# Performance work log

Hardware: AMD Instinct MI355X
Metric: run time of the kernel (lower is better)

## Reference

```python
import jax, jax.numpy as jnp
import numpy as np

N_NODES = 50000
ALPHA = 0.1
K_ITERS = 10


def setup_inputs() -> dict:
    key = jax.random.key(0)
    ks = jax.random.split(key, 6)
    x = jax.random.normal(ks[0], (N_NODES, 256), dtype=jnp.float32)
    edge_index = jax.random.randint(ks[1], (2, 800000), 0, N_NODES, dtype=jnp.int64)
    # Glorot-ish scaled weights
    W1 = jax.random.normal(ks[2], (256, 128), dtype=jnp.float32) * (1.0 / np.sqrt(256))
    b1 = jnp.zeros((128,), dtype=jnp.float32)
    W3 = jax.random.normal(ks[3], (128, 64), dtype=jnp.float32) * (1.0 / np.sqrt(128))
    b3 = jnp.zeros((64,), dtype=jnp.float32)
    return {"x": x, "edge_index": edge_index, "W1": W1, "b1": b1, "W3": W3, "b3": b3}


def _gcn_norm(edge_index, n_nodes):
    # Add self-loops, then symmetric normalization D^{-1/2} (A+I) D^{-1/2}
    loops = jnp.arange(n_nodes, dtype=edge_index.dtype)
    src = jnp.concatenate([edge_index[0], loops])
    dst = jnp.concatenate([edge_index[1], loops])
    deg = jax.ops.segment_sum(jnp.ones_like(dst, dtype=jnp.float32), dst,
                              num_segments=n_nodes)
    dinv = jnp.where(deg > 0, jax.lax.rsqrt(deg), 0.0)
    w = dinv[src] * dinv[dst]  # [E + N]
    return src, dst, w


def _propagate(h, src, dst, w, n_nodes):
    # out[dst] += w * h[src]  (gather -> scale -> scatter-add)
    msgs = w[:, None] * h[src]
    return jax.ops.segment_sum(msgs, dst, num_segments=n_nodes)


def reference(x, edge_index, W1, b1, W3, b3):
    n = x.shape[0]
    src, dst, w = _gcn_norm(edge_index, n)

    # GCNConv 1: linear then normalized propagation
    h = _propagate(x @ W1 + b1, src, dst, w, n)

    # APPNP: K iterations of h = (1-alpha)*A_hat h + alpha*h0 (eval: no edge dropout)
    h0 = h

    def step(hc, _):
        hn = (1.0 - ALPHA) * _propagate(hc, src, dst, w, n) + ALPHA * h0
        return hn, None

    h, _ = jax.lax.scan(step, h, None, length=K_ITERS)

    # GCNConv 2
    out = _propagate(h @ W3 + b3, src, dst, w, n)
    return out
```

## Files before the change

kernel.cpp:

```cpp
#include <hip/hip_runtime.h>

#define NN 50000
#define NE 800000
#define NTP (NE + 8 * NN)


__global__ void zero_deg_kernel(int* deg) {
  int v = blockIdx.x * 256 + threadIdx.x;
  if (v < NN) deg[v] = 0;
}

__global__ void count_deg_kernel(const int* __restrict__ edst, int* __restrict__ deg) {
  int i = blockIdx.x * 256 + threadIdx.x;
  if (i < NE) atomicAdd(&deg[edst[i]], 1);
}

__global__ void dinv_kernel(const int* __restrict__ deg, float* __restrict__ dinv) {
  int v = blockIdx.x * 256 + threadIdx.x;
  if (v < NN) dinv[v] = rsqrtf((float)(deg[v] + 1));
}

__device__ __forceinline__ int pdeg_of(int deg) {
  return ((deg + 8) >> 3) << 3;
}

__global__ __launch_bounds__(1024) void scan1_kernel(const int* __restrict__ deg,
                                                     int* __restrict__ incl,
                                                     int* __restrict__ bsum) {
  __shared__ int sd[1024];
  int gid = blockIdx.x * 1024 + threadIdx.x;
  int v = (gid < NN) ? pdeg_of(deg[gid]) : 0;
  sd[threadIdx.x] = v;
  __syncthreads();
  for (int off = 1; off < 1024; off <<= 1) {
    int t = (threadIdx.x >= off) ? sd[threadIdx.x - off] : 0;
    __syncthreads();
    sd[threadIdx.x] += t;
    __syncthreads();
  }
  if (gid < NN) incl[gid] = sd[threadIdx.x];
  if (threadIdx.x == 1023) bsum[blockIdx.x] = sd[1023];
}

__global__ void scan2_kernel(int* bsum, int nb) {
  if (threadIdx.x == 0 && blockIdx.x == 0) {
    int run = 0;
    for (int i = 0; i < nb; ++i) { int t = bsum[i]; bsum[i] = run; run += t; }
  }
}

__global__ void scan3_kernel(const int* __restrict__ deg, const int* __restrict__ incl,
                             const int* __restrict__ bsum, int* __restrict__ offs,
                             int* __restrict__ cursor) {
  int v = blockIdx.x * 256 + threadIdx.x;
  if (v >= NN) return;
  int pd = pdeg_of(deg[v]);
  int o = bsum[v >> 10] + incl[v] - pd;
  offs[v] = o;
  cursor[v] = o;
  if (v == NN - 1) offs[NN] = o + pd;
}

__global__ void zero_edges_kernel(int2* edges) {
  int i = blockIdx.x * 256 + threadIdx.x;
  if (i < NTP) edges[i] = make_int2(0, 0);
}

#define FILL_STRIDE (832 * 256)
__global__ void fill_kernel(const int* __restrict__ esrc, const int* __restrict__ edst,
                            const float* __restrict__ dinv, int* __restrict__ cursor,
                            int2* __restrict__ edges) {
  int i = blockIdx.x * 256 + threadIdx.x;
  for (; i < NE + NN; i += FILL_STRIDE) {
    int s, d;
    if (i < NE) { s = esrc[i]; d = edst[i]; }
    else        { s = d = i - NE; }
    int p = atomicAdd(&cursor[d], 1);
    int2 e;
    e.x = s;
    e.y = __float_as_int(dinv[s] * dinv[d]);
    edges[p] = e;
  }
}

__global__ void rowsum_kernel(const int* __restrict__ offs, const int2* __restrict__ edges,
                              float* __restrict__ rowsum) {
  int v = blockIdx.x * 256 + threadIdx.x;
  if (v >= NN) return;
  float s = 0.f;
  int e1 = offs[v + 1];
  for (int e = offs[v]; e < e1; ++e) s += __int_as_float(edges[e].y);
  rowsum[v] = s;
}


__global__ void w13_kernel(const float* __restrict__ W1, const float* __restrict__ W3,
                           float* __restrict__ W13) {
  int idx = blockIdx.x * 256 + threadIdx.x;
  if (idx >= 256 * 64) return;
  int r = idx >> 6, c = idx & 63;
  float acc = 0.f;
  for (int k = 0; k < 128; ++k) acc += W1[r * 128 + k] * W3[k * 64 + c];
  W13[idx] = acc;
}

__global__ void b13_kernel(const float* __restrict__ b1, const float* __restrict__ W3,
                           float* __restrict__ b13) {
  int c = threadIdx.x;
  if (c >= 64) return;
  float acc = 0.f;
  for (int k = 0; k < 128; ++k) acc += b1[k] * W3[k * 64 + c];
  b13[c] = acc;
}


template <int K>
__global__ __launch_bounds__(512) void gemm64_kernel(const float* __restrict__ A,
                                                     const float* __restrict__ W,
                                                     const float* __restrict__ bias,
                                                     float* __restrict__ out, int M) {
  __shared__ float xs[64][36];
  __shared__ float ws[32][64];

  int tid = threadIdx.x;
  int tc = tid & 15;
  int tr = tid >> 4;
  int row0 = blockIdx.x * 64;

  int xr = tid >> 3, xk = (tid & 7) * 4;
  int wk = tid >> 4, wc = (tid & 15) * 4;

  float acc[2][4] = {};

  for (int kc = 0; kc < K; kc += 32) {
    {
      int row = row0 + xr;
      float4 v = make_float4(0.f, 0.f, 0.f, 0.f);
      if (row < M) v = *reinterpret_cast<const float4*>(&A[(size_t)row * K + kc + xk]);
      *reinterpret_cast<float4*>(&xs[xr][xk]) = v;
      *reinterpret_cast<float4*>(&ws[wk][wc]) =
          *reinterpret_cast<const float4*>(&W[(size_t)(kc + wk) * 64 + wc]);
    }
    __syncthreads();
#pragma unroll
    for (int kk = 0; kk < 32; kk += 4) {
      float4 xv[2], wv[4];
#pragma unroll
      for (int r = 0; r < 2; ++r)
        xv[r] = *reinterpret_cast<const float4*>(&xs[tr * 2 + r][kk]);
#pragma unroll
      for (int q = 0; q < 4; ++q)
        wv[q] = *reinterpret_cast<const float4*>(&ws[kk + q][tc * 4]);
#pragma unroll
      for (int r = 0; r < 2; ++r) {
        acc[r][0] += xv[r].x * wv[0].x + xv[r].y * wv[1].x + xv[r].z * wv[2].x + xv[r].w * wv[3].x;
        acc[r][1] += xv[r].x * wv[0].y + xv[r].y * wv[1].y + xv[r].z * wv[2].y + xv[r].w * wv[3].y;
        acc[r][2] += xv[r].x * wv[0].z + xv[r].y * wv[1].z + xv[r].z * wv[2].z + xv[r].w * wv[3].z;
        acc[r][3] += xv[r].x * wv[0].w + xv[r].y * wv[1].w + xv[r].z * wv[2].w + xv[r].w * wv[3].w;
      }
    }
    __syncthreads();
  }

  float4 bv = *reinterpret_cast<const float4*>(&bias[tc * 4]);
#pragma unroll
  for (int r = 0; r < 2; ++r) {
    int row = row0 + tr * 2 + r;
    if (row < M) {
      float4 o;
      o.x = acc[r][0] + bv.x;
      o.y = acc[r][1] + bv.y;
      o.z = acc[r][2] + bv.z;
      o.w = acc[r][3] + bv.w;
      *reinterpret_cast<float4*>(&out[(size_t)row * 64 + tc * 4]) = o;
    }
  }
}


template <int MODE>
__global__ __launch_bounds__(256) void prop64_kernel(const float* __restrict__ hin,
                                                     const float* __restrict__ h0,
                                                     float* __restrict__ out,
                                                     const int* __restrict__ offs,
                                                     const int2* __restrict__ edges,
                                                     const float* __restrict__ rowsum,
                                                     const float* __restrict__ b3) {
  int node = blockIdx.x * 16 + (threadIdx.x >> 4);
  if (node >= NN) return;
  int f = (threadIdx.x & 15) * 4;
  const float* __restrict__ hb = hin + f;

  int e = offs[node];
  int e1 = offs[node + 1];
  float ax = 0.f, ay = 0.f, az = 0.f, aw = 0.f;

  for (; e < e1; e += 8) {
    int4 m01 = *reinterpret_cast<const int4*>(edges + e);
    int4 m23 = *reinterpret_cast<const int4*>(edges + e + 2);
    int4 m45 = *reinterpret_cast<const int4*>(edges + e + 4);
    int4 m67 = *reinterpret_cast<const int4*>(edges + e + 6);
    float4 v0 = *reinterpret_cast<const float4*>(hb + (size_t)m01.x * 64);
    float4 v1 = *reinterpret_cast<const float4*>(hb + (size_t)m01.z * 64);
    float4 v2 = *reinterpret_cast<const float4*>(hb + (size_t)m23.x * 64);
    float4 v3 = *reinterpret_cast<const float4*>(hb + (size_t)m23.z * 64);
    float4 v4 = *reinterpret_cast<const float4*>(hb + (size_t)m45.x * 64);
    float4 v5 = *reinterpret_cast<const float4*>(hb + (size_t)m45.z * 64);
    float4 v6 = *reinterpret_cast<const float4*>(hb + (size_t)m67.x * 64);
    float4 v7 = *reinterpret_cast<const float4*>(hb + (size_t)m67.z * 64);
    float w0 = __int_as_float(m01.y), w1 = __int_as_float(m01.w);
    float w2 = __int_as_float(m23.y), w3 = __int_as_float(m23.w);
    float w4 = __int_as_float(m45.y), w5 = __int_as_float(m45.w);
    float w6 = __int_as_float(m67.y), w7 = __int_as_float(m67.w);
    ax += w0 * v0.x + w1 * v1.x + w2 * v2.x + w3 * v3.x
        + w4 * v4.x + w5 * v5.x + w6 * v6.x + w7 * v7.x;
    ay += w0 * v0.y + w1 * v1.y + w2 * v2.y + w3 * v3.y
        + w4 * v4.y + w5 * v5.y + w6 * v6.y + w7 * v7.y;
    az += w0 * v0.z + w1 * v1.z + w2 * v2.z + w3 * v3.z
        + w4 * v4.z + w5 * v5.z + w6 * v6.z + w7 * v7.z;
    aw += w0 * v0.w + w1 * v1.w + w2 * v2.w + w3 * v3.w
        + w4 * v4.w + w5 * v5.w + w6 * v6.w + w7 * v7.w;
  }

  if (MODE == 1) {
    float4 z = *reinterpret_cast<const float4*>(&h0[(size_t)node * 64 + f]);
    ax = 0.9f * ax + 0.1f * z.x;
    ay = 0.9f * ay + 0.1f * z.y;
    az = 0.9f * az + 0.1f * z.z;
    aw = 0.9f * aw + 0.1f * z.w;
  }
  if (MODE == 2) {
    float rs = rowsum[node];
    float4 bz = *reinterpret_cast<const float4*>(&b3[f]);
    ax += rs * bz.x; ay += rs * bz.y; az += rs * bz.z; aw += rs * bz.w;
  }
  float4 o = make_float4(ax, ay, az, aw);
  *reinterpret_cast<float4*>(&out[(size_t)node * 64 + f]) = o;
}


extern "C" void kernel_launch(void* const* d_in, const int* in_sizes, int n_in,
                              void* d_out, int out_size, void* d_ws, size_t ws_size,
                              hipStream_t stream) {
  const float* x    = (const float*)d_in[0];
  const int*   eidx = (const int*)d_in[1];
  const float* W1   = (const float*)d_in[2];
  const float* b1   = (const float*)d_in[3];
  const float* W3   = (const float*)d_in[4];
  const float* b3   = (const float*)d_in[5];
  float* outp = (float*)d_out;

  const int* esrc = eidx;
  const int* edst = eidx + NE;

  char* w = (char*)d_ws;
  size_t off = 0;
  auto take = [&](size_t bytes) {
    void* p = w + off;
    off = (off + bytes + 255) & ~(size_t)255;
    return p;
  };
  int*   deg    = (int*)take(NN * 4);
  float* dinv   = (float*)take(NN * 4);
  int*   incl   = (int*)take(NN * 4);
  int*   offs   = (int*)take((NN + 1) * 4);
  int*   cursor = (int*)take(NN * 4);
  int*   bsum   = (int*)take(64 * 4);
  float* rsum   = (float*)take(NN * 4);
  float* W13    = (float*)take(256 * 64 * 4);
  float* b13    = (float*)take(64 * 4);
  int2*  edges  = (int2*)take((size_t)NTP * 8);
  float* y0     = (float*)take((size_t)NN * 64 * 4);
  float* z0     = (float*)take((size_t)NN * 64 * 4);
  float* zp     = (float*)take((size_t)NN * 64 * 4);
  float* zq     = (float*)take((size_t)NN * 64 * 4);
  (void)ws_size; (void)in_sizes; (void)n_in; (void)out_size;

  const int nblkN = (NN + 255) / 256;
  const int nblkE = (NE + 255) / 256;
  const int nblkP = (NTP + 255) / 256;
  const int nbScan = (NN + 1023) / 1024;

  w13_kernel<<<64, 256, 0, stream>>>(W1, W3, W13);
  b13_kernel<<<1, 64, 0, stream>>>(b1, W3, b13);

  zero_deg_kernel<<<nblkN, 256, 0, stream>>>(deg);
  count_deg_kernel<<<nblkE, 256, 0, stream>>>(edst, deg);
  dinv_kernel<<<nblkN, 256, 0, stream>>>(deg, dinv);
  scan1_kernel<<<nbScan, 1024, 0, stream>>>(deg, incl, bsum);
  scan2_kernel<<<1, 64, 0, stream>>>(bsum, nbScan);
  scan3_kernel<<<nblkN, 256, 0, stream>>>(deg, incl, bsum, offs, cursor);
  zero_edges_kernel<<<nblkP, 256, 0, stream>>>(edges);
  fill_kernel<<<832, 256, 0, stream>>>(esrc, edst, dinv, cursor, edges);
  rowsum_kernel<<<nblkN, 256, 0, stream>>>(offs, edges, rsum);

  gemm64_kernel<256><<<(NN + 63) / 64, 512, 0, stream>>>(x, W13, b13, y0, NN);

  const int pblk = (NN + 15) / 16;

  prop64_kernel<0><<<pblk, 256, 0, stream>>>(y0, nullptr, z0, offs, edges, nullptr, nullptr);

  const float* hc = z0;
  float* bufs[2] = {zp, zq};
  for (int it = 0; it < 10; ++it) {
    float* hn = bufs[it & 1];
    prop64_kernel<1><<<pblk, 256, 0, stream>>>(hc, z0, hn, offs, edges, nullptr, nullptr);
    hc = hn;
  }

  prop64_kernel<2><<<pblk, 256, 0, stream>>>(hc, nullptr, outp, offs, edges, rsum, b3);
}
```

Measured before the change: 511.5 us.

## Split 64-wide features into four 16-column slices for cache-local propagation

Stores the GEMM output and intermediate propagation buffers as four feature slices of 16 columns each. The propagation kernel then runs each block over one slice and one half of the nodes, so each block gathers 64-byte rows whose working set (about 3.2 MB per slice) can stay resident in L2/LLC. Edge, h0 and output accesses switch to nontemporal loads and stores so streaming data does not evict the gathered slice. The cost is that the edge list is re-read four times per iteration, and stores become scalar 4-byte writes instead of float4.

```diff
diff --git a/kernel.cpp b/kernel.cpp
--- a/kernel.cpp
+++ b/kernel.cpp
@@ -3,6 +3,8 @@
 #define NN 50000
 #define NE 800000
 #define NTP (NE + 8 * NN)
+#define SLICE_ST ((size_t)NN * 16)
+#define NHALF 25000
 
 
 __global__ void zero_deg_kernel(int* deg) {
@@ -163,6 +165,8 @@
   }
 
   float4 bv = *reinterpret_cast<const float4*>(&bias[tc * 4]);
+  int c0 = tc * 4;
+  float* obase = out + (size_t)(c0 >> 4) * SLICE_ST + (c0 & 15);
 #pragma unroll
   for (int r = 0; r < 2; ++r) {
     int row = row0 + tr * 2 + r;
@@ -172,70 +176,73 @@
       o.y = acc[r][1] + bv.y;
       o.z = acc[r][2] + bv.z;
       o.w = acc[r][3] + bv.w;
-      *reinterpret_cast<float4*>(&out[(size_t)row * 64 + tc * 4]) = o;
+      *reinterpret_cast<float4*>(obase + (size_t)row * 16) = o;
     }
   }
 }
 
 
 template <int MODE>
-__global__ __launch_bounds__(256) void prop64_kernel(const float* __restrict__ hin,
-                                                     const float* __restrict__ h0,
-                                                     float* __restrict__ out,
-                                                     const int* __restrict__ offs,
-                                                     const int2* __restrict__ edges,
-                                                     const float* __restrict__ rowsum,
-                                                     const float* __restrict__ b3) {
-  int node = blockIdx.x * 16 + (threadIdx.x >> 4);
-  if (node >= NN) return;
-  int f = (threadIdx.x & 15) * 4;
-  const float* __restrict__ hb = hin + f;
+__global__ __launch_bounds__(256) void propS_kernel(const float* __restrict__ hin,
+                                                    const float* __restrict__ h0,
+                                                    float* __restrict__ out,
+                                                    const int* __restrict__ offs,
+                                                    const int2* __restrict__ edges,
+                                                    const float* __restrict__ rowsum,
+                                                    const float* __restrict__ b3) {
+  int g8 = blockIdx.x & 7;
+  int slice = g8 & 3;
+  int half = g8 >> 2;
+  int node = half * NHALF + (int)(blockIdx.x >> 3) * 64 + (threadIdx.x >> 2);
+  if (node >= half * NHALF + NHALF) return;
+  int l4 = (threadIdx.x & 3) * 4;
+
+  const float* __restrict__ hs = hin + (size_t)slice * SLICE_ST + l4;
+  const long long* __restrict__ ell = reinterpret_cast<const long long*>(edges);
 
   int e = offs[node];
   int e1 = offs[node + 1];
   float ax = 0.f, ay = 0.f, az = 0.f, aw = 0.f;
 
   for (; e < e1; e += 8) {
-    int4 m01 = *reinterpret_cast<const int4*>(edges + e);
-    int4 m23 = *reinterpret_cast<const int4*>(edges + e + 2);
-    int4 m45 = *reinterpret_cast<const int4*>(edges + e + 4);
-    int4 m67 = *reinterpret_cast<const int4*>(edges + e + 6);
-    float4 v0 = *reinterpret_cast<const float4*>(hb + (size_t)m01.x * 64);
-    float4 v1 = *reinterpret_cast<const float4*>(hb + (size_t)m01.z * 64);
-    float4 v2 = *reinterpret_cast<const float4*>(hb + (size_t)m23.x * 64);
-    float4 v3 = *reinterpret_cast<const float4*>(hb + (size_t)m23.z * 64);
-    float4 v4 = *reinterpret_cast<const float4*>(hb + (size_t)m45.x * 64);
-    float4 v5 = *reinterpret_cast<const float4*>(hb + (size_t)m45.z * 64);
-    float4 v6 = *reinterpret_cast<const float4*>(hb + (size_t)m67.x * 64);
-    float4 v7 = *reinterpret_cast<const float4*>(hb + (size_t)m67.z * 64);
-    float w0 = __int_as_float(m01.y), w1 = __int_as_float(m01.w);
-    float w2 = __int_as_float(m23.y), w3 = __int_as_float(m23.w);
-    float w4 = __int_as_float(m45.y), w5 = __int_as_float(m45.w);
-    float w6 = __int_as_float(m67.y), w7 = __int_as_float(m67.w);
-    ax += w0 * v0.x + w1 * v1.x + w2 * v2.x + w3 * v3.x
-        + w4 * v4.x + w5 * v5.x + w6 * v6.x + w7 * v7.x;
-    ay += w0 * v0.y + w1 * v1.y + w2 * v2.y + w3 * v3.y
-        + w4 * v4.y + w5 * v5.y + w6 * v6.y + w7 * v7.y;
-    az += w0 * v0.z + w1 * v1.z + w2 * v2.z + w3 * v3.z
-        + w4 * v4.z + w5 * v5.z + w6 * v6.z + w7 * v7.z;
-    aw += w0 * v0.w + w1 * v1.w + w2 * v2.w + w3 * v3.w
-        + w4 * v4.w + w5 * v5.w + w6 * v6.w + w7 * v7.w;
+    long long m[8];
+#pragma unroll
+    for (int j = 0; j < 8; ++j) m[j] = __builtin_nontemporal_load(ell + e + j);
+    float4 v[8];
+#pragma unroll
+    for (int j = 0; j < 8; ++j)
+      v[j] = *reinterpret_cast<const float4*>(hs + (size_t)(int)m[j] * 16);
+#pragma unroll
+    for (int j = 0; j < 8; ++j) {
+      float wv = __int_as_float((int)(m[j] >> 32));
+      ax += wv * v[j].x; ay += wv * v[j].y; az += wv * v[j].z; aw += wv * v[j].w;
+    }
   }
 
   if (MODE == 1) {
-    float4 z = *reinterpret_cast<const float4*>(&h0[(size_t)node * 64 + f]);
-    ax = 0.9f * ax + 0.1f * z.x;
-    ay = 0.9f * ay + 0.1f * z.y;
-    az = 0.9f * az + 0.1f * z.z;
-    aw = 0.9f * aw + 0.1f * z.w;
-  }
+    const float* hz = h0 + (size_t)slice * SLICE_ST + (size_t)node * 16 + l4;
+    float zx = __builtin_nontemporal_load(hz + 0);
+    float zy = __builtin_nontemporal_load(hz + 1);
+    float zz = __builtin_nontemporal_load(hz + 2);
+    float zw = __builtin_nontemporal_load(hz + 3);
+    ax = 0.9f * ax + 0.1f * zx;
+    ay = 0.9f * ay + 0.1f * zy;
+    az = 0.9f * az + 0.1f * zz;
+    aw = 0.9f * aw + 0.1f * zw;
+  }
+  float* po;
   if (MODE == 2) {
     float rs = rowsum[node];
-    float4 bz = *reinterpret_cast<const float4*>(&b3[f]);
-    ax += rs * bz.x; ay += rs * bz.y; az += rs * bz.z; aw += rs * bz.w;
-  }
-  float4 o = make_float4(ax, ay, az, aw);
-  *reinterpret_cast<float4*>(&out[(size_t)node * 64 + f]) = o;
+    const float* bz = b3 + slice * 16 + l4;
+    ax += rs * bz[0]; ay += rs * bz[1]; az += rs * bz[2]; aw += rs * bz[3];
+    po = out + (size_t)node * 64 + slice * 16 + l4;
+  } else {
+    po = out + (size_t)slice * SLICE_ST + (size_t)node * 16 + l4;
+  }
+  __builtin_nontemporal_store(ax, po + 0);
+  __builtin_nontemporal_store(ay, po + 1);
+  __builtin_nontemporal_store(az, po + 2);
+  __builtin_nontemporal_store(aw, po + 3);
 }
 
 
@@ -296,17 +303,17 @@
 
   gemm64_kernel<256><<<(NN + 63) / 64, 512, 0, stream>>>(x, W13, b13, y0, NN);
 
-  const int pblk = (NN + 15) / 16;
-
-  prop64_kernel<0><<<pblk, 256, 0, stream>>>(y0, nullptr, z0, offs, edges, nullptr, nullptr);
+  const int pblkS = 8 * ((NHALF + 63) / 64);
+
+  propS_kernel<0><<<pblkS, 256, 0, stream>>>(y0, nullptr, z0, offs, edges, nullptr, nullptr);
 
   const float* hc = z0;
   float* bufs[2] = {zp, zq};
   for (int it = 0; it < 10; ++it) {
     float* hn = bufs[it & 1];
-    prop64_kernel<1><<<pblk, 256, 0, stream>>>(hc, z0, hn, offs, edges, nullptr, nullptr);
+    propS_kernel<1><<<pblkS, 256, 0, stream>>>(hc, z0, hn, offs, edges, nullptr, nullptr);
     hc = hn;
   }
 
-  prop64_kernel<2><<<pblk, 256, 0, stream>>>(hc, nullptr, outp, offs, edges, rsum, b3);
-}
+  propS_kernel<2><<<pblkS, 256, 0, stream>>>(hc, nullptr, outp, offs, edges, rsum, b3);
+}
```

After: 736.5 us. 1.44x slower.
